# Kernel optimization log

Hardware: AMD Instinct MI355X
Metric: run time of the kernel (lower is better)

## Reference

```python
import jax, jax.numpy as jnp
import numpy as np

B, S, HID, H, D = 4, 1024, 1024, 16, 64
MAXP = 1024  # max_position_embeddings
EPS = 1e-8


def setup_inputs() -> dict:
    key = jax.random.key(0)
    ks = jax.random.split(key, 9)
    scale = 0.02  # keep logits small since masked_softmax has no max-subtraction
    return {
        "hidden_states": jax.random.normal(ks[0], (B, S, HID), jnp.float32),
        "attention_mask": jnp.zeros((B, 1, 1, S), jnp.float32),
        "skim_mask": jax.random.randint(ks[1], (B, S), 0, 2, jnp.int32),
        "Wq": jax.random.normal(ks[2], (HID, HID), jnp.float32) * scale,
        "bq": jnp.zeros((HID,), jnp.float32),
        "Wk": jax.random.normal(ks[3], (HID, HID), jnp.float32) * scale,
        "bk": jnp.zeros((HID,), jnp.float32),
        "Wv": jax.random.normal(ks[4], (HID, HID), jnp.float32) * scale,
        "bv": jnp.zeros((HID,), jnp.float32),
        "dist_emb": jax.random.normal(ks[5], (2 * MAXP - 1, D), jnp.float32) * scale,
    }


def reference(hidden_states, attention_mask, skim_mask, Wq, bq, Wk, bk, Wv, bv, dist_emb):
    # Linear projections (W stored as [in, out]) then split heads: [B,H,S,D]
    def heads(x):
        return x.reshape(B, S, H, D).transpose(0, 2, 1, 3)

    q = heads(hidden_states @ Wq + bq)
    k = heads(hidden_states @ Wk + bk)
    v = heads(hidden_states @ Wv + bv)

    # raw scores [B,H,S,S]
    scores = jnp.einsum('bhld,bhrd->bhlr', q, k)

    # relative_key positional bias
    pos = jnp.arange(S)
    distance = pos[:, None] - pos[None, :]                 # [S,S]
    pe = dist_emb[distance + MAXP - 1]                     # [S,S,D]
    scores = scores + jnp.einsum('bhld,lrd->bhlr', q, pe)

    scores = scores / jnp.sqrt(jnp.float32(D))
    scores = scores + attention_mask

    # skim_mask branch: masked_softmax (exp * mask, normalized with eps)
    mask = skim_mask[:, None, None, :].astype(scores.dtype)  # [B,1,1,S]
    exps = jnp.exp(scores) * mask
    probs = exps / (EPS + exps.sum(-1, keepdims=True))
    # dropout in eval mode -> identity

    ctx = jnp.einsum('bhlr,bhrd->bhld', probs, v)
    return ctx.transpose(0, 2, 1, 3).reshape(B, S, HID)
```

## Files before the change

### kernel.cpp

```cpp
#include <hip/hip_runtime.h>
#include <hip/hip_bf16.h>


#define EPSV 1e-8f

typedef short bfrag __attribute__((ext_vector_type(8)));
typedef float cfrag __attribute__((ext_vector_type(16)));
typedef int v2i __attribute__((ext_vector_type(2)));

__device__ __forceinline__ short f2bf(float f) {
    __hip_bfloat16 h = __float2bfloat16(f);
    return *reinterpret_cast<short*>(&h);
}
__device__ __forceinline__ float bf2f(short s) {
    unsigned int u = ((unsigned int)(unsigned short)s) << 16;
    return __builtin_bit_cast(float, u);
}
__device__ __forceinline__ unsigned int pk2(short a, short b) {
    return (unsigned int)(unsigned short)a | ((unsigned int)(unsigned short)b << 16);
}

__global__ __launch_bounds__(256) void prep(
    const float* __restrict__ hidden, const float* __restrict__ Wq,
    const float* __restrict__ Wk, const float* __restrict__ Wv,
    const float* __restrict__ dist,
    short* __restrict__ Xs, short* __restrict__ Wt, short* __restrict__ Db)
{
    __shared__ short Tl[32 * 72];
    const int bid = blockIdx.x, tid = threadIdx.x;

    if (bid < 2048) {
        const int mt = bid >> 4, kg = bid & 15;
        const int m_l = tid >> 3, k8 = (tid & 7) * 8;
        const float* src = hidden + (size_t)(mt * 32 + m_l) * 1024 + kg * 64 + k8;
        float4 v0 = *(const float4*)src, v1 = *(const float4*)(src + 4);
        short o[8];
        o[0] = f2bf(v0.x); o[1] = f2bf(v0.y); o[2] = f2bf(v0.z); o[3] = f2bf(v0.w);
        o[4] = f2bf(v1.x); o[5] = f2bf(v1.y); o[6] = f2bf(v1.z); o[7] = f2bf(v1.w);
        *(bfrag*)&Tl[m_l * 72 + k8] = *(bfrag*)o;
        __syncthreads();
        const int l31 = tid & 31, q2 = (tid >> 5) & 1, kc = tid >> 6;
        bfrag r = *(const bfrag*)&Tl[l31 * 72 + kc * 16 + q2 * 8];
        *(bfrag*)(Xs + ((size_t)(mt * 64 + kg * 4 + kc) * 64 + q2 * 32 + l31) * 8) = r;
    } else if (bid < 3584) {
        const int t = bid - 2048, z = t >> 9, nt = (t >> 4) & 31, kg = t & 15;
        const float* W = (z == 0) ? Wq : ((z == 1) ? Wk : Wv);
        const int k_l = tid >> 2, n8 = (tid & 3) * 8;
        const float* src = W + (size_t)(kg * 64 + k_l) * 1024 + nt * 32 + n8;
        float4 v0 = *(const float4*)src, v1 = *(const float4*)(src + 4);
        float vv[8] = {v0.x, v0.y, v0.z, v0.w, v1.x, v1.y, v1.z, v1.w};
#pragma unroll
        for (int i = 0; i < 8; i++)
            Tl[(n8 + i) * 72 + k_l] = f2bf(vv[i]);
        __syncthreads();
        const int l31 = tid & 31, q2 = (tid >> 5) & 1, kc = tid >> 6;
        bfrag r = *(const bfrag*)&Tl[l31 * 72 + kc * 16 + q2 * 8];
        *(bfrag*)(Wt + (size_t)z * 1048576
                  + ((size_t)(nt * 64 + kg * 4 + kc) * 64 + q2 * 32 + l31) * 8) = r;
    } else {
        const int idx = (bid - 3584) * 256 + tid;
        if (idx < 16376) {
            const float* src = dist + (size_t)idx * 8;
            float4 v0 = *(const float4*)src, v1 = *(const float4*)(src + 4);
            short o[8];
            o[0] = f2bf(v0.x); o[1] = f2bf(v0.y); o[2] = f2bf(v0.z); o[3] = f2bf(v0.w);
            o[4] = f2bf(v1.x); o[5] = f2bf(v1.y); o[6] = f2bf(v1.z); o[7] = f2bf(v1.w);
            *(bfrag*)(Db + (size_t)idx * 8) = *(bfrag*)o;
        }
    }
}

__global__ __launch_bounds__(256) void qkv_mfma(
    const short* __restrict__ Xs, const short* __restrict__ Wt,
    const float* __restrict__ bq, const float* __restrict__ bk,
    const float* __restrict__ bv,
    short* __restrict__ Qf, short* __restrict__ Kf, short* __restrict__ Vt)
{
    const int z = blockIdx.z;
    const short* W = Wt + (size_t)z * 1048576;
    const float* bias = (z == 0) ? bq : ((z == 1) ? bk : bv);
    const float scale = (z == 0) ? 0.18033688011112042f : 1.0f;

    const int tid = threadIdx.x, lane = tid & 63, wid = tid >> 6;
    const int q2 = lane >> 5, l31 = lane & 31;
    const int wr = wid >> 1, wc = wid & 1;
    const int m0 = blockIdx.x * 128, n0 = blockIdx.y * 128;

    cfrag acc[2][2];
#pragma unroll
    for (int i = 0; i < 2; i++)
#pragma unroll
        for (int j = 0; j < 2; j++)
#pragma unroll
            for (int e = 0; e < 16; e++) acc[i][j][e] = 0.f;

    const short* ap0 = Xs + ((size_t)((m0 >> 5) + wr * 2 + 0) * 64 * 64 + lane) * 8;
    const short* ap1 = Xs + ((size_t)((m0 >> 5) + wr * 2 + 1) * 64 * 64 + lane) * 8;
    const short* bp0 = W  + ((size_t)((n0 >> 5) + wc * 2 + 0) * 64 * 64 + lane) * 8;
    const short* bp1 = W  + ((size_t)((n0 >> 5) + wc * 2 + 1) * 64 * 64 + lane) * 8;

#pragma unroll 4
    for (int kc = 0; kc < 64; kc++) {
        const int off = kc * 512;
        bfrag a0 = *(const bfrag*)(ap0 + off);
        bfrag a1 = *(const bfrag*)(ap1 + off);
        bfrag b0 = *(const bfrag*)(bp0 + off);
        bfrag b1 = *(const bfrag*)(bp1 + off);
        acc[0][0] = __builtin_amdgcn_mfma_f32_32x32x16_bf16(a0, b0, acc[0][0], 0, 0, 0);
        acc[0][1] = __builtin_amdgcn_mfma_f32_32x32x16_bf16(a0, b1, acc[0][1], 0, 0, 0);
        acc[1][0] = __builtin_amdgcn_mfma_f32_32x32x16_bf16(a1, b0, acc[1][0], 0, 0, 0);
        acc[1][1] = __builtin_amdgcn_mfma_f32_32x32x16_bf16(a1, b1, acc[1][1], 0, 0, 0);
    }

#pragma unroll
    for (int nt = 0; nt < 2; nt++) {
        const int c = n0 + wc * 64 + nt * 32 + l31;
        const float bval = bias[c];
        const int h = c >> 6;
        const int d = nt * 32 + l31;
#pragma unroll
        for (int mt = 0; mt < 2; mt++) {
            const int tok0 = m0 + wr * 64 + mt * 32;
            const int bb = tok0 >> 10, s_base = tok0 & 1023;
            const size_t bhbase = (size_t)(bb * 16 + h) * 65536;
            if (z < 2) {
                short* outp = (z == 0) ? Qf : Kf;
                const size_t fbase = bhbase
                    + ((size_t)((s_base >> 5) * 4 + (d >> 4)) * 64
                       + ((d >> 3) & 1) * 32) * 8 + (d & 7);
#pragma unroll
                for (int reg = 0; reg < 16; reg++) {
                    const int row = (reg & 3) + 8 * (reg >> 2) + 4 * q2;
                    outp[fbase + (size_t)row * 8] = f2bf((acc[mt][nt][reg] + bval) * scale);
                }
            } else {
#pragma unroll
                for (int g = 0; g < 4; g++) {
                    const float e0 = acc[mt][nt][4 * g + 0] + bval;
                    const float e1 = acc[mt][nt][4 * g + 1] + bval;
                    const float e2 = acc[mt][nt][4 * g + 2] + bval;
                    const float e3 = acc[mt][nt][4 * g + 3] + bval;
                    uint2 w2;
                    w2.x = pk2(f2bf(e0), f2bf(e1));
                    w2.y = pk2(f2bf(e2), f2bf(e3));
                    const size_t flat = bhbase
                        + ((size_t)(nt * 64 + (s_base >> 4) + (g >> 1)) * 64
                           + (g & 1) * 32 + l31) * 8 + 4 * q2;
                    *(uint2*)(Vt + flat) = w2;
                }
            }
        }
    }
}

__global__ __launch_bounds__(256, 2) void attn_mfma(
    const short* __restrict__ Qf, const short* __restrict__ Kf,
    const short* __restrict__ Vt, const short* __restrict__ Db,
    const float* __restrict__ amask, const int* __restrict__ skim,
    float* __restrict__ out)
{
    __shared__ short Tb[128 * 132];
    __shared__ float Lg[1024];

    const int tid = threadIdx.x, lane = tid & 63, w = tid >> 6;
    const int q2 = lane >> 5, l31 = lane & 31;
    const int bh = blockIdx.x, b = bh >> 4, hh = bh & 15;
    const int l0 = blockIdx.y * 128;

    {
        const int r4 = tid * 4;
        float4 am = *(const float4*)(amask + b * 1024 + r4);
        int4 sk = *(const int4*)(skim + b * 1024 + r4);
        Lg[r4 + 0] = __expf(am.x) * (float)sk.x;
        Lg[r4 + 1] = __expf(am.y) * (float)sk.y;
        Lg[r4 + 2] = __expf(am.z) * (float)sk.z;
        Lg[r4 + 3] = __expf(am.w) * (float)sk.w;
    }
    __syncthreads();

    const short* Qg = Qf + (size_t)bh * 65536;
    const short* Kg = Kf + (size_t)bh * 65536;
    const short* Vg = Vt + (size_t)bh * 65536;

    bfrag qa[4];
#pragma unroll
    for (int c = 0; c < 4; c++)
        qa[c] = *(const bfrag*)(Qg + ((size_t)(((l0 >> 5) + w) * 4 + c) * 64 + lane) * 8);

    cfrag oacc[2];
#pragma unroll
    for (int mt = 0; mt < 2; mt++)
#pragma unroll
        for (int e = 0; e < 16; e++) oacc[mt][e] = 0.f;
    float es[4] = {0.f, 0.f, 0.f, 0.f};

    const int Lband = l0 + 32 * w;
    const int lg = Lband + l31;
    const int rowb = (32 * w + l31) * 132;

    for (int r0 = -128; r0 < 1024; r0 += 64) {
        const bool produce = r0 < 960;

        bfrag pb[2][4];
        if (produce) {
#pragma unroll
            for (int mt = 0; mt < 2; mt++) {
                const int D0 = Lband - r0 - 128 + 32 * mt;
                const int er = min(max(D0 + l31 + 1023, 0), 2046);
#pragma unroll
                for (int kc = 0; kc < 4; kc++)
                    pb[mt][kc] = *(const bfrag*)(Db + (size_t)er * 64 + kc * 16 + q2 * 8);
            }
        }

        if (r0 >= 0) {
            bfrag kb[2][4], vbl[4][2];
#pragma unroll
            for (int mt = 0; mt < 2; mt++)
#pragma unroll
                for (int kc = 0; kc < 4; kc++)
                    kb[mt][kc] = *(const bfrag*)(Kg
                        + ((size_t)(((r0 >> 5) + mt) * 4 + kc) * 64 + lane) * 8);
#pragma unroll
            for (int kc = 0; kc < 4; kc++)
#pragma unroll
                for (int mtd = 0; mtd < 2; mtd++)
                    vbl[kc][mtd] = *(const bfrag*)(Vg
                        + ((size_t)(mtd * 64 + (r0 >> 4) + kc) * 64 + lane) * 8);

#pragma unroll
            for (int mt = 0; mt < 2; mt++) {
                cfrag sfr;
#pragma unroll
                for (int e = 0; e < 16; e++) sfr[e] = 0.f;
#pragma unroll
                for (int kc = 0; kc < 4; kc++)
                    sfr = __builtin_amdgcn_mfma_f32_32x32x16_bf16(
                        kb[mt][kc], qa[kc], sfr, 0, 0, 0);

                unsigned int P[4][2];
#pragma unroll
                for (int g = 0; g < 4; g++) {
                    const int rb = r0 + 32 * mt + 8 * g + 4 * q2;
                    float4 g4 = *(const float4*)&Lg[rb];
                    v2i tr = *(const v2i*)&Tb[rowb + (rb & 127)];
                    const float tv0 = __builtin_bit_cast(float, (unsigned)tr[0] << 16);
                    const float tv1 = __builtin_bit_cast(float, (unsigned)tr[0] & 0xffff0000u);
                    const float tv2 = __builtin_bit_cast(float, (unsigned)tr[1] << 16);
                    const float tv3 = __builtin_bit_cast(float, (unsigned)tr[1] & 0xffff0000u);
                    float ev0 = __builtin_amdgcn_exp2f(sfr[4 * g + 0] + tv0) * g4.x;
                    float ev1 = __builtin_amdgcn_exp2f(sfr[4 * g + 1] + tv1) * g4.y;
                    float ev2 = __builtin_amdgcn_exp2f(sfr[4 * g + 2] + tv2) * g4.z;
                    float ev3 = __builtin_amdgcn_exp2f(sfr[4 * g + 3] + tv3) * g4.w;
                    es[0] += ev0; es[1] += ev1; es[2] += ev2; es[3] += ev3;
                    P[g][0] = pk2(f2bf(ev0), f2bf(ev1));
                    P[g][1] = pk2(f2bf(ev2), f2bf(ev3));
                }
#pragma unroll
                for (int c = 0; c < 2; c++) {
                    v2i s0 = __builtin_amdgcn_permlane32_swap(
                        (int)P[2 * c][0], (int)P[2 * c + 1][0], false, false);
                    v2i s1 = __builtin_amdgcn_permlane32_swap(
                        (int)P[2 * c][1], (int)P[2 * c + 1][1], false, false);
                    union { bfrag f; int d[4]; } u;
                    u.d[0] = s0[0]; u.d[1] = s1[0]; u.d[2] = s0[1]; u.d[3] = s1[1];
                    const int kc = 2 * mt + c;
#pragma unroll
                    for (int mtd = 0; mtd < 2; mtd++)
                        oacc[mtd] = __builtin_amdgcn_mfma_f32_32x32x16_bf16(
                            vbl[kc][mtd], u.f, oacc[mtd], 0, 0, 0);
                }
            }
        }

        if (produce) {
#pragma unroll
            for (int mt = 0; mt < 2; mt++) {
                cfrag t;
#pragma unroll
                for (int e = 0; e < 16; e++) t[e] = 0.f;
#pragma unroll
                for (int kc = 0; kc < 4; kc++)
                    t = __builtin_amdgcn_mfma_f32_32x32x16_bf16(
                        pb[mt][kc], qa[kc], t, 0, 0, 0);
#pragma unroll
                for (int e = 0; e < 16; e++) {
                    const int rr = (e & 3) + 8 * (e >> 2) + 4 * q2;
                    Tb[rowb + ((l31 + r0 - 32 * mt - rr) & 127)] = f2bf(t[e]);
                }
            }
        }
    }

    float esum = (es[0] + es[1]) + (es[2] + es[3]);
    const float den = EPSV + esum + __shfl_xor(esum, 32);
    const float inv = 1.0f / den;
    float* ob = out + ((size_t)(b * 1024 + lg) * 1024) + hh * 64;
#pragma unroll
    for (int mtd = 0; mtd < 2; mtd++) {
#pragma unroll
        for (int g = 0; g < 4; g++) {
            float4 o;
            o.x = oacc[mtd][4 * g + 0] * inv;
            o.y = oacc[mtd][4 * g + 1] * inv;
            o.z = oacc[mtd][4 * g + 2] * inv;
            o.w = oacc[mtd][4 * g + 3] * inv;
            *(float4*)(ob + 32 * mtd + 8 * g + 4 * q2) = o;
        }
    }
}

extern "C" void kernel_launch(void* const* d_in, const int* in_sizes, int n_in,
                              void* d_out, int out_size, void* d_ws, size_t ws_size,
                              hipStream_t stream) {
    const float* hidden = (const float*)d_in[0];
    const float* amask  = (const float*)d_in[1];
    const int*   skim   = (const int*)d_in[2];
    const float* Wq     = (const float*)d_in[3];
    const float* bq     = (const float*)d_in[4];
    const float* Wk     = (const float*)d_in[5];
    const float* bk     = (const float*)d_in[6];
    const float* Wv     = (const float*)d_in[7];
    const float* bv     = (const float*)d_in[8];
    const float* dist   = (const float*)d_in[9];
    float* out = (float*)d_out;

    char* w = (char*)d_ws;
    short* Xs  = (short*)(w);
    short* Wt  = (short*)(w + ((size_t)8 << 20));
    short* Db  = (short*)(w + ((size_t)14 << 20));
    short* Qf  = (short*)(w + ((size_t)15 << 20));
    short* Kf  = (short*)(w + ((size_t)23 << 20));
    short* Vt  = (short*)(w + ((size_t)31 << 20));

    prep<<<3648, 256, 0, stream>>>(hidden, Wq, Wk, Wv, dist, Xs, Wt, Db);
    qkv_mfma<<<dim3(32, 8, 3), 256, 0, stream>>>(Xs, Wt, bq, bk, bv, Qf, Kf, Vt);
    attn_mfma<<<dim3(64, 8), 256, 0, stream>>>(Qf, Kf, Vt, Db, amask, skim, out);
}
```

Before: 196.2 us.

## Software-pipeline GEMM and attention loops with double-buffered fragment loads and MFMA priority

The projection GEMM inner loop now double-buffers its A/B fragment registers, so the next k-chunk loads are issued before the current MFMAs run. The attention loop is restructured into a manually pipelined schedule with ping-pong K fragment and Tb-row buffers, prefetching the next tile's K, positional-embedding and bias data while the current tile is consumed. MFMA groups are wrapped in s_setprio raises to favour matrix issue across waves. This aims to hide global and LDS load latency, at the cost of higher register pressure and possible occupancy loss.

```diff
diff --git a/kernel.cpp b/kernel.cpp
--- a/kernel.cpp
+++ b/kernel.cpp
@@ -11,10 +11,6 @@
 __device__ __forceinline__ short f2bf(float f) {
     __hip_bfloat16 h = __float2bfloat16(f);
     return *reinterpret_cast<short*>(&h);
-}
-__device__ __forceinline__ float bf2f(short s) {
-    unsigned int u = ((unsigned int)(unsigned short)s) << 16;
-    return __builtin_bit_cast(float, u);
 }
 __device__ __forceinline__ unsigned int pk2(short a, short b) {
     return (unsigned int)(unsigned short)a | ((unsigned int)(unsigned short)b << 16);
@@ -99,17 +95,30 @@
     const short* bp0 = W  + ((size_t)((n0 >> 5) + wc * 2 + 0) * 64 * 64 + lane) * 8;
     const short* bp1 = W  + ((size_t)((n0 >> 5) + wc * 2 + 1) * 64 * 64 + lane) * 8;
 
-#pragma unroll 4
-    for (int kc = 0; kc < 64; kc++) {
-        const int off = kc * 512;
-        bfrag a0 = *(const bfrag*)(ap0 + off);
-        bfrag a1 = *(const bfrag*)(ap1 + off);
-        bfrag b0 = *(const bfrag*)(bp0 + off);
-        bfrag b1 = *(const bfrag*)(bp1 + off);
-        acc[0][0] = __builtin_amdgcn_mfma_f32_32x32x16_bf16(a0, b0, acc[0][0], 0, 0, 0);
-        acc[0][1] = __builtin_amdgcn_mfma_f32_32x32x16_bf16(a0, b1, acc[0][1], 0, 0, 0);
-        acc[1][0] = __builtin_amdgcn_mfma_f32_32x32x16_bf16(a1, b0, acc[1][0], 0, 0, 0);
-        acc[1][1] = __builtin_amdgcn_mfma_f32_32x32x16_bf16(a1, b1, acc[1][1], 0, 0, 0);
+    bfrag a0c, a1c, b0c, b1c, a0n, a1n, b0n, b1n;
+    a0c = *(const bfrag*)(ap0); a1c = *(const bfrag*)(ap1);
+    b0c = *(const bfrag*)(bp0); b1c = *(const bfrag*)(bp1);
+
+#pragma unroll 2
+    for (int kc = 0; kc < 64; kc += 2) {
+        {
+            const int off = (kc + 1) * 512;
+            a0n = *(const bfrag*)(ap0 + off); a1n = *(const bfrag*)(ap1 + off);
+            b0n = *(const bfrag*)(bp0 + off); b1n = *(const bfrag*)(bp1 + off);
+        }
+        acc[0][0] = __builtin_amdgcn_mfma_f32_32x32x16_bf16(a0c, b0c, acc[0][0], 0, 0, 0);
+        acc[0][1] = __builtin_amdgcn_mfma_f32_32x32x16_bf16(a0c, b1c, acc[0][1], 0, 0, 0);
+        acc[1][0] = __builtin_amdgcn_mfma_f32_32x32x16_bf16(a1c, b0c, acc[1][0], 0, 0, 0);
+        acc[1][1] = __builtin_amdgcn_mfma_f32_32x32x16_bf16(a1c, b1c, acc[1][1], 0, 0, 0);
+        if (kc + 2 < 64) {
+            const int off = (kc + 2) * 512;
+            a0c = *(const bfrag*)(ap0 + off); a1c = *(const bfrag*)(ap1 + off);
+            b0c = *(const bfrag*)(bp0 + off); b1c = *(const bfrag*)(bp1 + off);
+        }
+        acc[0][0] = __builtin_amdgcn_mfma_f32_32x32x16_bf16(a0n, b0n, acc[0][0], 0, 0, 0);
+        acc[0][1] = __builtin_amdgcn_mfma_f32_32x32x16_bf16(a0n, b1n, acc[0][1], 0, 0, 0);
+        acc[1][0] = __builtin_amdgcn_mfma_f32_32x32x16_bf16(a1n, b0n, acc[1][0], 0, 0, 0);
+        acc[1][1] = __builtin_amdgcn_mfma_f32_32x32x16_bf16(a1n, b1n, acc[1][1], 0, 0, 0);
     }
 
 #pragma unroll
@@ -198,97 +207,126 @@
     const int lg = Lband + l31;
     const int rowb = (32 * w + l31) * 132;
 
-    for (int r0 = -128; r0 < 1024; r0 += 64) {
-        const bool produce = r0 < 960;
-
-        bfrag pb[2][4];
-        if (produce) {
-#pragma unroll
-            for (int mt = 0; mt < 2; mt++) {
-                const int D0 = Lband - r0 - 128 + 32 * mt;
-                const int er = min(max(D0 + l31 + 1023, 0), 2046);
-#pragma unroll
-                for (int kc = 0; kc < 4; kc++)
-                    pb[mt][kc] = *(const bfrag*)(Db + (size_t)er * 64 + kc * 16 + q2 * 8);
+    auto LOADPB = [&](int r0k, bfrag (&PB)[2][4]) {
+#pragma unroll
+        for (int mt = 0; mt < 2; mt++) {
+            const int er = min(max(Lband - r0k - 128 + 32 * mt + l31 + 1023, 0), 2046);
+#pragma unroll
+            for (int kc = 0; kc < 4; kc++)
+                PB[mt][kc] = *(const bfrag*)(Db + (size_t)er * 64 + kc * 16 + q2 * 8);
+        }
+    };
+    auto PRODUCE = [&](int r0k, bfrag (&PB)[2][4]) {
+#pragma unroll
+        for (int mt = 0; mt < 2; mt++) {
+            cfrag t;
+#pragma unroll
+            for (int e = 0; e < 16; e++) t[e] = 0.f;
+            __builtin_amdgcn_s_setprio(1);
+#pragma unroll
+            for (int kc = 0; kc < 4; kc++)
+                t = __builtin_amdgcn_mfma_f32_32x32x16_bf16(PB[mt][kc], qa[kc], t, 0, 0, 0);
+            __builtin_amdgcn_s_setprio(0);
+#pragma unroll
+            for (int e = 0; e < 16; e++) {
+                const int rr = (e & 3) + 8 * (e >> 2) + 4 * q2;
+                Tb[rowb + ((l31 + r0k - 32 * mt - rr) & 127)] = f2bf(t[e]);
             }
         }
-
-        if (r0 >= 0) {
-            bfrag kb[2][4], vbl[4][2];
-#pragma unroll
-            for (int mt = 0; mt < 2; mt++)
-#pragma unroll
-                for (int kc = 0; kc < 4; kc++)
-                    kb[mt][kc] = *(const bfrag*)(Kg
-                        + ((size_t)(((r0 >> 5) + mt) * 4 + kc) * 64 + lane) * 8);
+    };
+    auto LOADKB = [&](int r0k, bfrag (&KB)[2][4]) {
+#pragma unroll
+        for (int mt = 0; mt < 2; mt++)
 #pragma unroll
             for (int kc = 0; kc < 4; kc++)
+                KB[mt][kc] = *(const bfrag*)(Kg
+                    + ((size_t)(((r0k >> 5) + mt) * 4 + kc) * 64 + lane) * 8);
+    };
+    auto LOADTR = [&](int r0k, v2i (&TR)[8]) {
+#pragma unroll
+        for (int i = 0; i < 8; i++)
+            TR[i] = *(const v2i*)&Tb[rowb
+                + ((r0k + 32 * (i >> 2) + 8 * (i & 3) + 4 * q2) & 127)];
+    };
+    auto CONSUME = [&](int r0v, bfrag (&KB)[2][4], v2i (&TR)[8]) {
+#pragma unroll
+        for (int mt = 0; mt < 2; mt++) {
+            bfrag vbl[2][2];
+#pragma unroll
+            for (int c = 0; c < 2; c++)
 #pragma unroll
                 for (int mtd = 0; mtd < 2; mtd++)
-                    vbl[kc][mtd] = *(const bfrag*)(Vg
-                        + ((size_t)(mtd * 64 + (r0 >> 4) + kc) * 64 + lane) * 8);
-
-#pragma unroll
-            for (int mt = 0; mt < 2; mt++) {
-                cfrag sfr;
-#pragma unroll
-                for (int e = 0; e < 16; e++) sfr[e] = 0.f;
-#pragma unroll
-                for (int kc = 0; kc < 4; kc++)
-                    sfr = __builtin_amdgcn_mfma_f32_32x32x16_bf16(
-                        kb[mt][kc], qa[kc], sfr, 0, 0, 0);
-
-                unsigned int P[4][2];
-#pragma unroll
-                for (int g = 0; g < 4; g++) {
-                    const int rb = r0 + 32 * mt + 8 * g + 4 * q2;
-                    float4 g4 = *(const float4*)&Lg[rb];
-                    v2i tr = *(const v2i*)&Tb[rowb + (rb & 127)];
-                    const float tv0 = __builtin_bit_cast(float, (unsigned)tr[0] << 16);
-                    const float tv1 = __builtin_bit_cast(float, (unsigned)tr[0] & 0xffff0000u);
-                    const float tv2 = __builtin_bit_cast(float, (unsigned)tr[1] << 16);
-                    const float tv3 = __builtin_bit_cast(float, (unsigned)tr[1] & 0xffff0000u);
-                    float ev0 = __builtin_amdgcn_exp2f(sfr[4 * g + 0] + tv0) * g4.x;
-                    float ev1 = __builtin_amdgcn_exp2f(sfr[4 * g + 1] + tv1) * g4.y;
-                    float ev2 = __builtin_amdgcn_exp2f(sfr[4 * g + 2] + tv2) * g4.z;
-                    float ev3 = __builtin_amdgcn_exp2f(sfr[4 * g + 3] + tv3) * g4.w;
-                    es[0] += ev0; es[1] += ev1; es[2] += ev2; es[3] += ev3;
-                    P[g][0] = pk2(f2bf(ev0), f2bf(ev1));
-                    P[g][1] = pk2(f2bf(ev2), f2bf(ev3));
-                }
-#pragma unroll
-                for (int c = 0; c < 2; c++) {
-                    v2i s0 = __builtin_amdgcn_permlane32_swap(
-                        (int)P[2 * c][0], (int)P[2 * c + 1][0], false, false);
-                    v2i s1 = __builtin_amdgcn_permlane32_swap(
-                        (int)P[2 * c][1], (int)P[2 * c + 1][1], false, false);
-                    union { bfrag f; int d[4]; } u;
-                    u.d[0] = s0[0]; u.d[1] = s1[0]; u.d[2] = s0[1]; u.d[3] = s1[1];
-                    const int kc = 2 * mt + c;
-#pragma unroll
-                    for (int mtd = 0; mtd < 2; mtd++)
-                        oacc[mtd] = __builtin_amdgcn_mfma_f32_32x32x16_bf16(
-                            vbl[kc][mtd], u.f, oacc[mtd], 0, 0, 0);
-                }
+                    vbl[c][mtd] = *(const bfrag*)(Vg
+                        + ((size_t)(mtd * 64 + (r0v >> 4) + 2 * mt + c) * 64 + lane) * 8);
+            cfrag sfr;
+#pragma unroll
+            for (int e = 0; e < 16; e++) sfr[e] = 0.f;
+            __builtin_amdgcn_s_setprio(1);
+#pragma unroll
+            for (int kc = 0; kc < 4; kc++)
+                sfr = __builtin_amdgcn_mfma_f32_32x32x16_bf16(
+                    KB[mt][kc], qa[kc], sfr, 0, 0, 0);
+            __builtin_amdgcn_s_setprio(0);
+
+            unsigned int P[4][2];
+#pragma unroll
+            for (int g = 0; g < 4; g++) {
+                const int rb = r0v + 32 * mt + 8 * g + 4 * q2;
+                float4 g4 = *(const float4*)&Lg[rb];
+                v2i tr2 = TR[4 * mt + g];
+                const float tv0 = __builtin_bit_cast(float, (unsigned)tr2[0] << 16);
+                const float tv1 = __builtin_bit_cast(float, (unsigned)tr2[0] & 0xffff0000u);
+                const float tv2 = __builtin_bit_cast(float, (unsigned)tr2[1] << 16);
+                const float tv3 = __builtin_bit_cast(float, (unsigned)tr2[1] & 0xffff0000u);
+                float ev0 = __builtin_amdgcn_exp2f(sfr[4 * g + 0] + tv0) * g4.x;
+                float ev1 = __builtin_amdgcn_exp2f(sfr[4 * g + 1] + tv1) * g4.y;
+                float ev2 = __builtin_amdgcn_exp2f(sfr[4 * g + 2] + tv2) * g4.z;
+                float ev3 = __builtin_amdgcn_exp2f(sfr[4 * g + 3] + tv3) * g4.w;
+                es[0] += ev0; es[1] += ev1; es[2] += ev2; es[3] += ev3;
+                P[g][0] = pk2(f2bf(ev0), f2bf(ev1));
+                P[g][1] = pk2(f2bf(ev2), f2bf(ev3));
             }
-        }
-
-        if (produce) {
-#pragma unroll
-            for (int mt = 0; mt < 2; mt++) {
-                cfrag t;
-#pragma unroll
-                for (int e = 0; e < 16; e++) t[e] = 0.f;
-#pragma unroll
-                for (int kc = 0; kc < 4; kc++)
-                    t = __builtin_amdgcn_mfma_f32_32x32x16_bf16(
-                        pb[mt][kc], qa[kc], t, 0, 0, 0);
-#pragma unroll
-                for (int e = 0; e < 16; e++) {
-                    const int rr = (e & 3) + 8 * (e >> 2) + 4 * q2;
-                    Tb[rowb + ((l31 + r0 - 32 * mt - rr) & 127)] = f2bf(t[e]);
-                }
+#pragma unroll
+            for (int c = 0; c < 2; c++) {
+                v2i s0 = __builtin_amdgcn_permlane32_swap(
+                    (int)P[2 * c][0], (int)P[2 * c + 1][0], false, false);
+                v2i s1 = __builtin_amdgcn_permlane32_swap(
+                    (int)P[2 * c][1], (int)P[2 * c + 1][1], false, false);
+                union { bfrag f; int d[4]; } u;
+                u.d[0] = s0[0]; u.d[1] = s1[0]; u.d[2] = s0[1]; u.d[3] = s1[1];
+                __builtin_amdgcn_s_setprio(1);
+#pragma unroll
+                for (int mtd = 0; mtd < 2; mtd++)
+                    oacc[mtd] = __builtin_amdgcn_mfma_f32_32x32x16_bf16(
+                        vbl[c][mtd], u.f, oacc[mtd], 0, 0, 0);
+                __builtin_amdgcn_s_setprio(0);
             }
+        }
+    };
+
+    bfrag kbA[2][4], kbB[2][4], pb[2][4];
+    v2i trA[8], trB[8];
+
+    LOADPB(-128, pb);
+    LOADKB(0, kbA);
+    PRODUCE(-128, pb);
+    LOADPB(-64, pb);
+    PRODUCE(-64, pb);
+    LOADTR(0, trA);
+    LOADPB(0, pb);
+
+    for (int r0 = 0; r0 < 1024; r0 += 128) {
+        LOADKB(r0 + 64, kbB);
+        CONSUME(r0, kbA, trA);
+        PRODUCE(r0, pb);
+        LOADTR(r0 + 64, trB);
+        LOADPB(r0 + 64, pb);
+        if (r0 + 128 < 1024) LOADKB(r0 + 128, kbA);
+        CONSUME(r0 + 64, kbB, trB);
+        if (r0 + 64 < 960) {
+            PRODUCE(r0 + 64, pb);
+            LOADTR(r0 + 128, trA);
+            LOADPB(r0 + 128, pb);
         }
     }
 
```

Result: slower. 233.9 us (+19.2%).
